# Optimization experiments

Hardware: AMD Instinct MI355X
Metric: run time of the kernel (lower is better)

## Reference

```python
import jax, jax.numpy as jnp
import numpy as np

B, N, H = 32, 1024, 512
DT = 0.1  # euler step size = t[1]-t[0] for torchdiffeq euler on t=[0.0,0.1]

def setup_inputs() -> dict:
    key = jax.random.key(0)
    ks = jax.random.split(key, 8)
    s = 1.0 / np.sqrt(2 * H)
    return {
        "inp": jax.random.normal(ks[0], (B, N, H), jnp.float32),
        "hz": jax.random.normal(ks[1], (B, N, H), jnp.float32),
        # func1: tanh(Linear(2H -> 2H)) ODE dynamics
        "Wf": jax.random.uniform(ks[2], (2 * H, 2 * H), jnp.float32, -s, s),
        "bf": jnp.zeros((2 * H,), jnp.float32),
        # mlp head: Linear(2H,2H) -> ReLU -> Linear(2H,H) -> Tanh
        "W1": jax.random.uniform(ks[3], (2 * H, 2 * H), jnp.float32, -s, s),
        "b1": jnp.zeros((2 * H,), jnp.float32),
        "W2": jax.random.uniform(ks[4], (2 * H, H), jnp.float32, -s, s),
        "b2": jnp.zeros((H,), jnp.float32),
    }

def reference(inp, hz, Wf, bf, W1, b1, W2, b2):
    # h0 = cat([input, hz], -1)  -> [B, N, 2H]
    h = jnp.concatenate([inp, hz], axis=-1)
    def func1(h):  # dh/dt (time-independent dynamics)
        return jnp.tanh(h @ Wf + bf)
    # two odeint calls, each a single fixed euler step over t=[0.0, 0.1]
    for _ in range(2):
        h = h + DT * func1(h)
    # MLP head
    h = jax.nn.relu(h @ W1 + b1)
    h = jnp.tanh(h @ W2 + b2)
    return h  # [B, N, H]
```

## Files before the change

### kernel.cpp

```cpp
#include <hip/hip_runtime.h>
#include <hip/hip_bf16.h>

typedef __attribute__((ext_vector_type(8))) short short8;
typedef __attribute__((ext_vector_type(4))) float floatx4;

__device__ __forceinline__ ushort f2bf(float x) {
    __hip_bfloat16 h = __float2bfloat16(x);
    return __builtin_bit_cast(ushort, h);
}
__device__ __forceinline__ float bf2f(ushort u) {
    __hip_bfloat16 h = __builtin_bit_cast(__hip_bfloat16, u);
    return __bfloat162float(h);
}

__device__ __forceinline__ float fast_tanh(float z) {
    float e = __expf(2.0f * z);
    return 1.0f - 2.0f * __builtin_amdgcn_rcpf(e + 1.0f);
}

__device__ __forceinline__ void gload_lds16(const ushort* g, ushort* l) {
    __builtin_amdgcn_global_load_lds(
        (const __attribute__((address_space(1))) unsigned int*)(const void*)g,
        (__attribute__((address_space(3))) unsigned int*)(void*)l,
        16, 0, 0);
}

__global__ void prep(const float* __restrict__ inp, const float* __restrict__ hz,
                     const float* __restrict__ Wf, const float* __restrict__ W1,
                     const float* __restrict__ W2,
                     ushort* __restrict__ h0, ushort* __restrict__ WfT,
                     ushort* __restrict__ W1T, ushort* __restrict__ W2T) {
    int bid = blockIdx.x;
    int tid = threadIdx.x;
    __shared__ float tile[32][33];
    if (bid < 32768) {
        const float* src = (bid < 16384) ? inp : hz;
        int half = (bid < 16384) ? 0 : 1;
        int b = bid - half * 16384;
        size_t i = ((size_t)b * 256 + tid) * 4;
        size_t row = i >> 9;
        int col = (int)(i & 511);
        float4 v = *(const float4*)(src + i);
        ushort4 o = make_ushort4(f2bf(v.x), f2bf(v.y), f2bf(v.z), f2bf(v.w));
        *(ushort4*)(h0 + row * 1024 + half * 512 + col) = o;
    } else {
        int t = bid - 32768;
        const float* W;
        ushort* WT;
        int K = 1024, N = 1024;
        if (t < 1024)      { W = Wf; WT = WfT; }
        else if (t < 2048) { W = W1; WT = W1T; t -= 1024; }
        else               { W = W2; WT = W2T; t -= 2048; N = 512; }
        int tx = tid & 31, ty = tid >> 5;
        int nb = (t % (N / 32)) * 32, kb = (t / (N / 32)) * 32;
        #pragma unroll
        for (int j = ty; j < 32; j += 8)
            tile[j][tx] = W[(size_t)(kb + j) * N + nb + tx];
        __syncthreads();
        #pragma unroll
        for (int j = ty; j < 32; j += 8)
            WT[(size_t)(nb + j) * K + kb + tx] = f2bf(tile[tx][j]);
    }
}

template <int MODE, int NOUT, int NX>
__global__ __launch_bounds__(512, 2) void gemm_ep(
    const ushort* __restrict__ A, const ushort* __restrict__ BT,
    const float* __restrict__ bias,
    ushort* __restrict__ outB, float* __restrict__ outF) {
    constexpr int K = 1024;
    constexpr int NT = 32;
    __shared__ ushort As[4][128 * 32];
    __shared__ ushort Bs[4][256 * 32];

    const int tid = threadIdx.x;
    const int wave = tid >> 6, lane = tid & 63;

    const int id = blockIdx.x;
    const int inner = id >> 3;
    const int nTile = inner % NX;
    const int mTile = (id & 7) * 32 + inner / NX;
    const int mBase = mTile * 128;
    const int nBase = nTile * 256;
    const int waveM = wave >> 2;
    const int waveN = wave & 3;

    const int ca = wave * 64 + lane;
    const int ra = ca >> 2;
    const int qa = (ca & 3) ^ ((ra >> 1) & 3);
    const ushort* agA = A + (size_t)(mBase + ra) * K + qa * 8;
    const ushort* bg0 = BT + (size_t)(nBase + ra) * K + qa * 8;
    const ushort* bg1 = BT + (size_t)(nBase + ra + 128) * K + qa * 8;
    ushort* asD  = &As[0][0] + (size_t)(wave * 64) * 8;
    ushort* bsD0 = &Bs[0][0] + (size_t)(wave * 64) * 8;
    ushort* bsD1 = &Bs[0][0] + (size_t)(wave * 64 + 512) * 8;

    floatx4 acc[4][4];
    #pragma unroll
    for (int i = 0; i < 4; i++)
        #pragma unroll
        for (int j = 0; j < 4; j++) acc[i][j] = (floatx4)(0.f);

    const int mrow = lane & 15;
    const int g = lane >> 4;
    const int pq = g ^ ((mrow >> 1) & 3);
    const int kqOff = pq * 8;

    const ushort* aB = &As[0][0] + (waveM * 64 + mrow) * 32 + kqOff;
    const ushort* bB = &Bs[0][0] + (waveN * 64 + mrow) * 32 + kqOff;

    #define STAGE(t) do {                                          \
        const int s_ = (t) & 3;                                    \
        gload_lds16(agA + (t) * 32, asD  + s_ * 4096);             \
        gload_lds16(bg0 + (t) * 32, bsD0 + s_ * 8192);             \
        gload_lds16(bg1 + (t) * 32, bsD1 + s_ * 8192);             \
    } while (0)

    STAGE(0); STAGE(1); STAGE(2);
    asm volatile("s_waitcnt vmcnt(6)" ::: "memory");
    __builtin_amdgcn_s_barrier();

    #pragma unroll
    for (int t = 0; t < NT; ++t) {
        const int s = t & 3;
        short8 af[4], bfr[4];
        #pragma unroll
        for (int i = 0; i < 4; i++) {
            af[i]  = *(const short8*)(aB + s * 4096 + i * 512);
            bfr[i] = *(const short8*)(bB + s * 8192 + i * 512);
        }
        if (t + 3 < NT) {
            STAGE(t + 3);
            asm volatile("s_waitcnt vmcnt(6)" ::: "memory");
        } else {
            asm volatile("s_waitcnt vmcnt(0)" ::: "memory");
        }
        __builtin_amdgcn_s_barrier();
        asm volatile("s_waitcnt lgkmcnt(0)" ::: "memory");
        __builtin_amdgcn_sched_barrier(0);
        __builtin_amdgcn_s_setprio(1);
        #pragma unroll
        for (int mt = 0; mt < 4; mt++)
            #pragma unroll
            for (int nt = 0; nt < 4; nt++)
                acc[mt][nt] = __builtin_amdgcn_mfma_f32_16x16x32_bf16(
                    af[mt], bfr[nt], acc[mt][nt], 0, 0, 0);
        __builtin_amdgcn_s_setprio(0);
        __builtin_amdgcn_sched_barrier(0);
        __builtin_amdgcn_s_barrier();
    }
    #undef STAGE

    const int col0 = nBase + waveN * 64 + (lane & 15);
    const int row0 = mBase + waveM * 64 + (lane >> 4) * 4;
    #pragma unroll
    for (int mt = 0; mt < 4; mt++) {
        #pragma unroll
        for (int nt = 0; nt < 4; nt++) {
            const int col = col0 + nt * 16;
            const float bv = bias[col];
            #pragma unroll
            for (int r = 0; r < 4; r++) {
                const int row = row0 + mt * 16 + r;
                const float z = acc[mt][nt][r] + bv;
                if (MODE == 1) {
                    float carry = bf2f(A[(size_t)row * K + col]);
                    outB[(size_t)row * NOUT + col] = f2bf(carry + 0.1f * fast_tanh(z));
                } else if (MODE == 2) {
                    outB[(size_t)row * NOUT + col] = f2bf(fmaxf(z, 0.f));
                } else {
                    outF[(size_t)row * NOUT + col] = fast_tanh(z);
                }
            }
        }
    }
}

extern "C" void kernel_launch(void* const* d_in, const int* in_sizes, int n_in,
                              void* d_out, int out_size, void* d_ws, size_t ws_size,
                              hipStream_t stream) {
    const float* inp = (const float*)d_in[0];
    const float* hz  = (const float*)d_in[1];
    const float* Wf  = (const float*)d_in[2];
    const float* bf_ = (const float*)d_in[3];
    const float* W1  = (const float*)d_in[4];
    const float* b1  = (const float*)d_in[5];
    const float* W2  = (const float*)d_in[6];
    const float* b2  = (const float*)d_in[7];
    float* out = (float*)d_out;

    char* ws = (char*)d_ws;
    ushort* WfT  = (ushort*)(ws);
    ushort* W1T  = (ushort*)(ws + (size_t)(2 << 20));
    ushort* W2T  = (ushort*)(ws + (size_t)(4 << 20));
    ushort* bufA = (ushort*)(ws + (size_t)(8 << 20));
    ushort* bufB = (ushort*)(ws + (size_t)(8 << 20) + ((size_t)64 << 20));

    prep<<<35328, 256, 0, stream>>>(inp, hz, Wf, W1, W2, bufA, WfT, W1T, W2T);

    gemm_ep<1, 1024, 4><<<1024, 512, 0, stream>>>(bufA, WfT, bf_, bufB, nullptr);
    gemm_ep<1, 1024, 4><<<1024, 512, 0, stream>>>(bufB, WfT, bf_, bufA, nullptr);
    gemm_ep<2, 1024, 4><<<1024, 512, 0, stream>>>(bufA, W1T, b1, bufB, nullptr);
    gemm_ep<3, 512, 2><<<512, 512, 0, stream>>>(bufB, W2T, b2, nullptr, out);
}
```

Measured before the change: 507.5 us.

## Enlarge GEMM block tile to 256x256 with split half-panel MFMA pipeline

Doubles the M dimension of each block tile from 128 to 256 rows, so each wave computes a 128x64 sub-tile with 8x4 accumulators and the grid shrinks by half. Each K-panel is split into two halves whose global-to-LDS loads are interleaved between the MFMA groups, with hand-tuned vmcnt waits. The aim is more reuse of each B tile and a higher ratio of MFMA work to loads. In exchange it uses more registers and LDS, which may cut occupancy below two blocks per CU, and it adds extra barriers per panel.

```diff
diff --git a/kernel.cpp b/kernel.cpp
--- a/kernel.cpp
+++ b/kernel.cpp
@@ -69,9 +69,8 @@
     const float* __restrict__ bias,
     ushort* __restrict__ outB, float* __restrict__ outF) {
     constexpr int K = 1024;
-    constexpr int NT = 32;
-    __shared__ ushort As[4][128 * 32];
-    __shared__ ushort Bs[4][256 * 32];
+    __shared__ ushort As[4][8192];
+    __shared__ ushort Bs[4][8192];
 
     const int tid = threadIdx.x;
     const int wave = tid >> 6, lane = tid & 63;
@@ -79,82 +78,114 @@
     const int id = blockIdx.x;
     const int inner = id >> 3;
     const int nTile = inner % NX;
-    const int mTile = (id & 7) * 32 + inner / NX;
-    const int mBase = mTile * 128;
+    const int mTile = (id & 7) * 16 + inner / NX;
+    const int mBase = mTile * 256;
     const int nBase = nTile * 256;
     const int waveM = wave >> 2;
     const int waveN = wave & 3;
 
-    const int ca = wave * 64 + lane;
-    const int ra = ca >> 2;
-    const int qa = (ca & 3) ^ ((ra >> 1) & 3);
-    const ushort* agA = A + (size_t)(mBase + ra) * K + qa * 8;
-    const ushort* bg0 = BT + (size_t)(nBase + ra) * K + qa * 8;
-    const ushort* bg1 = BT + (size_t)(nBase + ra + 128) * K + qa * 8;
-    ushort* asD  = &As[0][0] + (size_t)(wave * 64) * 8;
-    ushort* bsD0 = &Bs[0][0] + (size_t)(wave * 64) * 8;
-    ushort* bsD1 = &Bs[0][0] + (size_t)(wave * 64 + 512) * 8;
-
-    floatx4 acc[4][4];
+    const int c = wave * 64 + lane;
+    const int ra = c >> 2;
+    const int qa = (c & 3) ^ ((ra >> 1) & 3);
+    const ushort* agA0 = A  + (size_t)(mBase + ra) * K + qa * 8;
+    const ushort* agA1 = A  + (size_t)(mBase + 128 + ra) * K + qa * 8;
+    const ushort* bgB0 = BT + (size_t)(nBase + ra) * K + qa * 8;
+    const ushort* bgB1 = BT + (size_t)(nBase + 128 + ra) * K + qa * 8;
+    ushort* asD = &As[0][0] + wave * 512;
+    ushort* bsD = &Bs[0][0] + wave * 512;
+
+    floatx4 acc[8][4];
     #pragma unroll
-    for (int i = 0; i < 4; i++)
+    for (int i = 0; i < 8; i++)
         #pragma unroll
         for (int j = 0; j < 4; j++) acc[i][j] = (floatx4)(0.f);
 
     const int mrow = lane & 15;
     const int g = lane >> 4;
     const int pq = g ^ ((mrow >> 1) & 3);
-    const int kqOff = pq * 8;
-
-    const ushort* aB = &As[0][0] + (waveM * 64 + mrow) * 32 + kqOff;
-    const ushort* bB = &Bs[0][0] + (waveN * 64 + mrow) * 32 + kqOff;
-
-    #define STAGE(t) do {                                          \
-        const int s_ = (t) & 3;                                    \
-        gload_lds16(agA + (t) * 32, asD  + s_ * 4096);             \
-        gload_lds16(bg0 + (t) * 32, bsD0 + s_ * 8192);             \
-        gload_lds16(bg1 + (t) * 32, bsD1 + s_ * 8192);             \
-    } while (0)
-
-    STAGE(0); STAGE(1); STAGE(2);
-    asm volatile("s_waitcnt vmcnt(6)" ::: "memory");
+    const ushort* aB = &As[0][0] + (waveM * 128 + mrow) * 32 + pq * 8;
+    const ushort* bB = &Bs[0][0] + (waveN * 64 + mrow) * 32 + pq * 8;
+
+#define MFMA_ROW(MT, AF)                                                            \
+    acc[MT][0] = __builtin_amdgcn_mfma_f32_16x16x32_bf16(AF, bf0, acc[MT][0], 0,0,0); \
+    acc[MT][1] = __builtin_amdgcn_mfma_f32_16x16x32_bf16(AF, bf1, acc[MT][1], 0,0,0); \
+    acc[MT][2] = __builtin_amdgcn_mfma_f32_16x16x32_bf16(AF, bf2, acc[MT][2], 0,0,0); \
+    acc[MT][3] = __builtin_amdgcn_mfma_f32_16x16x32_bf16(AF, bf3, acc[MT][3], 0,0,0);
+
+#define PANEL(T, STG, VMASM)                                                   \
+  {                                                                            \
+    const int s  = (T) & 3;                                                    \
+    const int s3 = ((T) + 3) & 3;                                              \
+                \
+    short8 af0 = *(const short8*)(aB + s * 8192 + 0 * 512);                    \
+    short8 af1 = *(const short8*)(aB + s * 8192 + 1 * 512);                    \
+    short8 af2 = *(const short8*)(aB + s * 8192 + 2 * 512);                    \
+    short8 af3 = *(const short8*)(aB + s * 8192 + 3 * 512);                    \
+    short8 bf0 = *(const short8*)(bB + s * 8192 + 0 * 512);                    \
+    short8 bf1 = *(const short8*)(bB + s * 8192 + 1 * 512);                    \
+    short8 bf2 = *(const short8*)(bB + s * 8192 + 2 * 512);                    \
+    short8 bf3 = *(const short8*)(bB + s * 8192 + 3 * 512);                    \
+    if (STG) {                                                                 \
+      gload_lds16(agA0 + ((T) + 3) * 32, asD + s3 * 8192);                     \
+      gload_lds16(agA1 + ((T) + 3) * 32, asD + s3 * 8192 + 4096);              \
+    }                                                                          \
+    __builtin_amdgcn_s_barrier();                                              \
+    asm volatile("s_waitcnt lgkmcnt(0)" ::: "memory");                         \
+    __builtin_amdgcn_sched_barrier(0);                                         \
+    __builtin_amdgcn_s_setprio(1);                                             \
+    MFMA_ROW(0, af0) MFMA_ROW(1, af1) MFMA_ROW(2, af2) MFMA_ROW(3, af3)        \
+    __builtin_amdgcn_s_setprio(0);                                             \
+    __builtin_amdgcn_sched_barrier(0);                                         \
+    __builtin_amdgcn_s_barrier();                                              \
+          \
+    af0 = *(const short8*)(aB + s * 8192 + 2048 + 0 * 512);                    \
+    af1 = *(const short8*)(aB + s * 8192 + 2048 + 1 * 512);                    \
+    af2 = *(const short8*)(aB + s * 8192 + 2048 + 2 * 512);                    \
+    af3 = *(const short8*)(aB + s * 8192 + 2048 + 3 * 512);                    \
+    if (STG) {                                                                 \
+      gload_lds16(bgB0 + ((T) + 3) * 32, bsD + s3 * 8192);                     \
+      gload_lds16(bgB1 + ((T) + 3) * 32, bsD + s3 * 8192 + 4096);              \
+    }                                                                          \
+    asm volatile(VMASM ::: "memory");                                          \
+    __builtin_amdgcn_s_barrier();                                              \
+    asm volatile("s_waitcnt lgkmcnt(0)" ::: "memory");                         \
+    __builtin_amdgcn_sched_barrier(0);                                         \
+    __builtin_amdgcn_s_setprio(1);                                             \
+    MFMA_ROW(4, af0) MFMA_ROW(5, af1) MFMA_ROW(6, af2) MFMA_ROW(7, af3)        \
+    __builtin_amdgcn_s_setprio(0);                                             \
+    __builtin_amdgcn_sched_barrier(0);                                         \
+    __builtin_amdgcn_s_barrier();                                              \
+  }
+
+    #pragma unroll
+    for (int p = 0; p < 3; ++p) {
+        gload_lds16(agA0 + p * 32, asD + p * 8192);
+        gload_lds16(agA1 + p * 32, asD + p * 8192 + 4096);
+        gload_lds16(bgB0 + p * 32, bsD + p * 8192);
+        gload_lds16(bgB1 + p * 32, bsD + p * 8192 + 4096);
+    }
+    asm volatile("s_waitcnt vmcnt(8)" ::: "memory");
     __builtin_amdgcn_s_barrier();
 
+    for (int tt = 0; tt < 7; ++tt) {
+        const int t4 = tt * 4;
+        PANEL(t4 + 0, true, "s_waitcnt vmcnt(8)")
+        PANEL(t4 + 1, true, "s_waitcnt vmcnt(8)")
+        PANEL(t4 + 2, true, "s_waitcnt vmcnt(8)")
+        PANEL(t4 + 3, true, "s_waitcnt vmcnt(8)")
+    }
+    PANEL(28, true,  "s_waitcnt vmcnt(8)")
+    PANEL(29, false, "s_waitcnt vmcnt(4)")
+    PANEL(30, false, "s_waitcnt vmcnt(0)")
+    PANEL(31, false, "s_waitcnt vmcnt(0)")
+
+#undef PANEL
+#undef MFMA_ROW
+
+    const int col0 = nBase + waveN * 64 + (lane & 15);
+    const int row0 = mBase + waveM * 128 + (lane >> 4) * 4;
     #pragma unroll
-    for (int t = 0; t < NT; ++t) {
-        const int s = t & 3;
-        short8 af[4], bfr[4];
-        #pragma unroll
-        for (int i = 0; i < 4; i++) {
-            af[i]  = *(const short8*)(aB + s * 4096 + i * 512);
-            bfr[i] = *(const short8*)(bB + s * 8192 + i * 512);
-        }
-        if (t + 3 < NT) {
-            STAGE(t + 3);
-            asm volatile("s_waitcnt vmcnt(6)" ::: "memory");
-        } else {
-            asm volatile("s_waitcnt vmcnt(0)" ::: "memory");
-        }
-        __builtin_amdgcn_s_barrier();
-        asm volatile("s_waitcnt lgkmcnt(0)" ::: "memory");
-        __builtin_amdgcn_sched_barrier(0);
-        __builtin_amdgcn_s_setprio(1);
-        #pragma unroll
-        for (int mt = 0; mt < 4; mt++)
-            #pragma unroll
-            for (int nt = 0; nt < 4; nt++)
-                acc[mt][nt] = __builtin_amdgcn_mfma_f32_16x16x32_bf16(
-                    af[mt], bfr[nt], acc[mt][nt], 0, 0, 0);
-        __builtin_amdgcn_s_setprio(0);
-        __builtin_amdgcn_sched_barrier(0);
-        __builtin_amdgcn_s_barrier();
-    }
-    #undef STAGE
-
-    const int col0 = nBase + waveN * 64 + (lane & 15);
-    const int row0 = mBase + waveM * 64 + (lane >> 4) * 4;
-    #pragma unroll
-    for (int mt = 0; mt < 4; mt++) {
+    for (int mt = 0; mt < 8; mt++) {
         #pragma unroll
         for (int nt = 0; nt < 4; nt++) {
             const int col = col0 + nt * 16;
@@ -198,8 +229,8 @@
 
     prep<<<35328, 256, 0, stream>>>(inp, hz, Wf, W1, W2, bufA, WfT, W1T, W2T);
 
-    gemm_ep<1, 1024, 4><<<1024, 512, 0, stream>>>(bufA, WfT, bf_, bufB, nullptr);
-    gemm_ep<1, 1024, 4><<<1024, 512, 0, stream>>>(bufB, WfT, bf_, bufA, nullptr);
-    gemm_ep<2, 1024, 4><<<1024, 512, 0, stream>>>(bufA, W1T, b1, bufB, nullptr);
-    gemm_ep<3, 512, 2><<<512, 512, 0, stream>>>(bufB, W2T, b2, nullptr, out);
-}
+    gemm_ep<1, 1024, 4><<<512, 512, 0, stream>>>(bufA, WfT, bf_, bufB, nullptr);
+    gemm_ep<1, 1024, 4><<<512, 512, 0, stream>>>(bufB, WfT, bf_, bufA, nullptr);
+    gemm_ep<2, 1024, 4><<<512, 512, 0, stream>>>(bufA, W1T, b1, bufB, nullptr);
+    gemm_ep<3, 512, 2><<<256, 512, 0, stream>>>(bufB, W2T, b2, nullptr, out);
+}
```

After: 448.5 us. 11.6% less time.

## Shrink GEMM tile to 128x128 with double buffering and widen prep stores

Applied to the files above, without the earlier changes.

The GEMM kernel moves from a 128x256 tile with 512 threads and a 4-stage LDS ring to a 128x128 tile with 256 threads and 2-stage double buffering. Grids double in size and launch bounds now target 3 blocks per CU. The hand-placed waitcnt and sched barriers are replaced by plain __syncthreads. The prep kernel now converts 8 floats per thread and writes 8-byte transposed weight stores. The smaller tiles give less reuse per block and a shallower prefetch pipeline in exchange for more blocks resident per CU.

```diff
diff --git a/kernel.cpp b/kernel.cpp
--- a/kernel.cpp
+++ b/kernel.cpp
@@ -33,45 +33,53 @@
     int bid = blockIdx.x;
     int tid = threadIdx.x;
     __shared__ float tile[32][33];
-    if (bid < 32768) {
-        const float* src = (bid < 16384) ? inp : hz;
-        int half = (bid < 16384) ? 0 : 1;
-        int b = bid - half * 16384;
-        size_t i = ((size_t)b * 256 + tid) * 4;
-        size_t row = i >> 9;
-        int col = (int)(i & 511);
-        float4 v = *(const float4*)(src + i);
-        ushort4 o = make_ushort4(f2bf(v.x), f2bf(v.y), f2bf(v.z), f2bf(v.w));
-        *(ushort4*)(h0 + row * 1024 + half * 512 + col) = o;
+    if (bid < 16384) {
+        int u = bid * 256 + tid;
+        const int isHz = (u >= 2097152) ? 1 : 0;
+        const float* src = isHz ? hz : inp;
+        const int v = u - isHz * 2097152;
+        const size_t i = (size_t)v * 8;
+        const size_t row = i >> 9;
+        const int col = (int)(i & 511);
+        float4 x0 = *(const float4*)(src + i);
+        float4 x1 = *(const float4*)(src + i + 4);
+        short8 o;
+        o[0] = (short)f2bf(x0.x); o[1] = (short)f2bf(x0.y);
+        o[2] = (short)f2bf(x0.z); o[3] = (short)f2bf(x0.w);
+        o[4] = (short)f2bf(x1.x); o[5] = (short)f2bf(x1.y);
+        o[6] = (short)f2bf(x1.z); o[7] = (short)f2bf(x1.w);
+        *(short8*)(h0 + row * 1024 + isHz * 512 + col) = o;
     } else {
-        int t = bid - 32768;
+        int t = bid - 16384;
         const float* W;
         ushort* WT;
-        int K = 1024, N = 1024;
+        int N = 1024;
         if (t < 1024)      { W = Wf; WT = WfT; }
         else if (t < 2048) { W = W1; WT = W1T; t -= 1024; }
         else               { W = W2; WT = W2T; t -= 2048; N = 512; }
-        int tx = tid & 31, ty = tid >> 5;
-        int nb = (t % (N / 32)) * 32, kb = (t / (N / 32)) * 32;
+        const int tx = tid & 31, ty = tid >> 5;
+        const int nb = (t % (N / 32)) * 32, kb = (t / (N / 32)) * 32;
         #pragma unroll
         for (int j = ty; j < 32; j += 8)
             tile[j][tx] = W[(size_t)(kb + j) * N + nb + tx];
         __syncthreads();
-        #pragma unroll
-        for (int j = ty; j < 32; j += 8)
-            WT[(size_t)(nb + j) * K + kb + tx] = f2bf(tile[tx][j]);
+        const int j2 = tid >> 3;
+        const int kc = (tid & 7) * 4;
+        ushort4 o = make_ushort4(f2bf(tile[kc][j2]),     f2bf(tile[kc + 1][j2]),
+                                 f2bf(tile[kc + 2][j2]), f2bf(tile[kc + 3][j2]));
+        *(ushort4*)(WT + (size_t)(nb + j2) * 1024 + kb + kc) = o;
     }
 }
 
 template <int MODE, int NOUT, int NX>
-__global__ __launch_bounds__(512, 2) void gemm_ep(
+__global__ __launch_bounds__(256, 3) void gemm_ep(
     const ushort* __restrict__ A, const ushort* __restrict__ BT,
     const float* __restrict__ bias,
     ushort* __restrict__ outB, float* __restrict__ outF) {
     constexpr int K = 1024;
     constexpr int NT = 32;
-    __shared__ ushort As[4][128 * 32];
-    __shared__ ushort Bs[4][256 * 32];
+    __shared__ ushort As[2][4096];
+    __shared__ ushort Bs[2][4096];
 
     const int tid = threadIdx.x;
     const int wave = tid >> 6, lane = tid & 63;
@@ -81,19 +89,18 @@
     const int nTile = inner % NX;
     const int mTile = (id & 7) * 32 + inner / NX;
     const int mBase = mTile * 128;
-    const int nBase = nTile * 256;
-    const int waveM = wave >> 2;
-    const int waveN = wave & 3;
-
-    const int ca = wave * 64 + lane;
-    const int ra = ca >> 2;
-    const int qa = (ca & 3) ^ ((ra >> 1) & 3);
-    const ushort* agA = A + (size_t)(mBase + ra) * K + qa * 8;
-    const ushort* bg0 = BT + (size_t)(nBase + ra) * K + qa * 8;
-    const ushort* bg1 = BT + (size_t)(nBase + ra + 128) * K + qa * 8;
-    ushort* asD  = &As[0][0] + (size_t)(wave * 64) * 8;
-    ushort* bsD0 = &Bs[0][0] + (size_t)(wave * 64) * 8;
-    ushort* bsD1 = &Bs[0][0] + (size_t)(wave * 64 + 512) * 8;
+    const int nBase = nTile * 128;
+    const int waveM = wave >> 1;
+    const int waveN = wave & 1;
+
+    const int c0 = tid, c1 = tid + 256;
+    const int ra0 = c0 >> 2, ra1 = c1 >> 2;
+    const int qa0 = (c0 & 3) ^ ((ra0 >> 1) & 3);
+    const int qa1 = (c1 & 3) ^ ((ra1 >> 1) & 3);
+    const ushort* agA_0 = A  + (size_t)(mBase + ra0) * K + qa0 * 8;
+    const ushort* agA_1 = A  + (size_t)(mBase + ra1) * K + qa1 * 8;
+    const ushort* bgB_0 = BT + (size_t)(nBase + ra0) * K + qa0 * 8;
+    const ushort* bgB_1 = BT + (size_t)(nBase + ra1) * K + qa1 * 8;
 
     floatx4 acc[4][4];
     #pragma unroll
@@ -104,40 +111,31 @@
     const int mrow = lane & 15;
     const int g = lane >> 4;
     const int pq = g ^ ((mrow >> 1) & 3);
-    const int kqOff = pq * 8;
-
-    const ushort* aB = &As[0][0] + (waveM * 64 + mrow) * 32 + kqOff;
-    const ushort* bB = &Bs[0][0] + (waveN * 64 + mrow) * 32 + kqOff;
-
-    #define STAGE(t) do {                                          \
-        const int s_ = (t) & 3;                                    \
-        gload_lds16(agA + (t) * 32, asD  + s_ * 4096);             \
-        gload_lds16(bg0 + (t) * 32, bsD0 + s_ * 8192);             \
-        gload_lds16(bg1 + (t) * 32, bsD1 + s_ * 8192);             \
-    } while (0)
-
-    STAGE(0); STAGE(1); STAGE(2);
-    asm volatile("s_waitcnt vmcnt(6)" ::: "memory");
-    __builtin_amdgcn_s_barrier();
-
-    #pragma unroll
+    const ushort* aB = &As[0][0] + (waveM * 64 + mrow) * 32 + pq * 8;
+    const ushort* bB = &Bs[0][0] + (waveN * 64 + mrow) * 32 + pq * 8;
+
+#define STAGE(T)                                                        \
+    {                                                                   \
+        const int s_ = (T) & 1;                                         \
+        gload_lds16(agA_0 + (T) * 32, &As[s_][0] + tid * 8);            \
+        gload_lds16(agA_1 + (T) * 32, &As[s_][0] + (tid + 256) * 8);    \
+        gload_lds16(bgB_0 + (T) * 32, &Bs[s_][0] + tid * 8);            \
+        gload_lds16(bgB_1 + (T) * 32, &Bs[s_][0] + (tid + 256) * 8);    \
+    }
+
+    STAGE(0)
+    __syncthreads();
+
+    #pragma unroll 4
     for (int t = 0; t < NT; ++t) {
-        const int s = t & 3;
+        const int s = t & 1;
+        if (t + 1 < NT) STAGE(t + 1)
         short8 af[4], bfr[4];
         #pragma unroll
         for (int i = 0; i < 4; i++) {
             af[i]  = *(const short8*)(aB + s * 4096 + i * 512);
-            bfr[i] = *(const short8*)(bB + s * 8192 + i * 512);
+            bfr[i] = *(const short8*)(bB + s * 4096 + i * 512);
         }
-        if (t + 3 < NT) {
-            STAGE(t + 3);
-            asm volatile("s_waitcnt vmcnt(6)" ::: "memory");
-        } else {
-            asm volatile("s_waitcnt vmcnt(0)" ::: "memory");
-        }
-        __builtin_amdgcn_s_barrier();
-        asm volatile("s_waitcnt lgkmcnt(0)" ::: "memory");
-        __builtin_amdgcn_sched_barrier(0);
         __builtin_amdgcn_s_setprio(1);
         #pragma unroll
         for (int mt = 0; mt < 4; mt++)
@@ -146,10 +144,9 @@
                 acc[mt][nt] = __builtin_amdgcn_mfma_f32_16x16x32_bf16(
                     af[mt], bfr[nt], acc[mt][nt], 0, 0, 0);
         __builtin_amdgcn_s_setprio(0);
-        __builtin_amdgcn_sched_barrier(0);
-        __builtin_amdgcn_s_barrier();
-    }
-    #undef STAGE
+        __syncthreads();
+    }
+#undef STAGE
 
     const int col0 = nBase + waveN * 64 + (lane & 15);
     const int row0 = mBase + waveM * 64 + (lane >> 4) * 4;
@@ -196,10 +193,10 @@
     ushort* bufA = (ushort*)(ws + (size_t)(8 << 20));
     ushort* bufB = (ushort*)(ws + (size_t)(8 << 20) + ((size_t)64 << 20));
 
-    prep<<<35328, 256, 0, stream>>>(inp, hz, Wf, W1, W2, bufA, WfT, W1T, W2T);
-
-    gemm_ep<1, 1024, 4><<<1024, 512, 0, stream>>>(bufA, WfT, bf_, bufB, nullptr);
-    gemm_ep<1, 1024, 4><<<1024, 512, 0, stream>>>(bufB, WfT, bf_, bufA, nullptr);
-    gemm_ep<2, 1024, 4><<<1024, 512, 0, stream>>>(bufA, W1T, b1, bufB, nullptr);
-    gemm_ep<3, 512, 2><<<512, 512, 0, stream>>>(bufB, W2T, b2, nullptr, out);
-}
+    prep<<<18944, 256, 0, stream>>>(inp, hz, Wf, W1, W2, bufA, WfT, W1T, W2T);
+
+    gemm_ep<1, 1024, 8><<<2048, 256, 0, stream>>>(bufA, WfT, bf_, bufB, nullptr);
+    gemm_ep<1, 1024, 8><<<2048, 256, 0, stream>>>(bufB, WfT, bf_, bufA, nullptr);
+    gemm_ep<2, 1024, 8><<<2048, 256, 0, stream>>>(bufA, W1T, b1, bufB, nullptr);
+    gemm_ep<3, 512, 4><<<1024, 256, 0, stream>>>(bufB, W2T, b2, nullptr, out);
+}
```

Result: faster. 484.5 us (-4.5%).
